# Kernel tuning notes

Measured on AMD Instinct MI355X. Metric: run time of the kernel, lower is better.

The kernel has to match this reference:

```python
import jax, jax.numpy as jnp
import numpy as np

BATCH = 64
NUM_BEAMS = 16
VOCAB = 128000
CUR_LEN = 8


def setup_inputs() -> dict:
    key = jax.random.key(0)
    k1, k2, k3 = jax.random.split(key, 3)
    rows = BATCH * NUM_BEAMS
    logits = jax.random.normal(k1, (rows, 1, VOCAB), dtype=jnp.float32)
    decoder_input_ids = jax.random.randint(k2, (rows, CUR_LEN), 0, VOCAB, dtype=jnp.int32)
    # mid-decode beam scores: arbitrary (negative-ish) cumulative log-probs
    beam_scores = jax.random.normal(k3, (rows,), dtype=jnp.float32)
    # arange(batch).repeat_interleave(num_beams) * num_beams
    beam_idx_offset = jnp.repeat(jnp.arange(BATCH, dtype=jnp.int32), NUM_BEAMS) * NUM_BEAMS
    return {
        "logits": logits,
        "decoder_input_ids": decoder_input_ids,
        "beam_scores": beam_scores,
        "beam_idx_offset": beam_idx_offset,
        "batch_size": BATCH,
        "num_beams": NUM_BEAMS,
    }


def reference(logits, decoder_input_ids, beam_scores, beam_idx_offset, batch_size, num_beams):
    # logits: [batch*beams, seq, vocab]; only the last position is used.
    vocab_size = logits.shape[-1]
    next_token_scores = jax.nn.log_softmax(logits[:, -1, :], axis=-1)  # [B*K, V]
    next_token_scores = next_token_scores + beam_scores[:, None]
    next_token_scores = next_token_scores.reshape(batch_size, num_beams * vocab_size)
    # top 2*K over the joint (beam, vocab) axis, sorted descending
    top_scores, top_idx = jax.lax.top_k(next_token_scores, 2 * num_beams)
    next_indices = top_idx // vocab_size  # source beam within batch
    next_tokens = top_idx % vocab_size    # token id
    new_beam_scores = top_scores[:, :num_beams].reshape(-1)           # [B*K]
    beam_next_tokens = next_tokens[:, :num_beams].reshape(-1)         # [B*K]
    beam_idx = next_indices[:, :num_beams].reshape(-1)                # [B*K]
    gathered = decoder_input_ids[beam_idx + beam_idx_offset, :]       # reorder beams
    new_decoder_input_ids = jnp.concatenate(
        [gathered, beam_next_tokens[:, None].astype(gathered.dtype)], axis=-1
    )
    return new_decoder_input_ids, new_beam_scores
```

## Files before the change

kernel.cpp:

```cpp
#include <hip/hip_runtime.h>
#include <cfloat>
#include <climits>

#define ROWS    1024
#define VOCABSZ 128000
#define NBEAMS  16
#define NBATCH  64
#define CURLEN  8
#define KTOP    16
#define WPB     4
#define NSTEP   125
#define TCAP    128
#define TGUARD  112
#define RCAP    768
#define RFLUSH  508
#define LOG2E   1.4426950408889634f
#define LN2     0.6931471805599453f
#define THRY    (3.30f * LOG2E)

#if __has_builtin(__builtin_amdgcn_exp2f)
#define EXP2(x) __builtin_amdgcn_exp2f(x)
#else
#define EXP2(x) exp2f(x)
#endif

__global__ __launch_bounds__(256) void k1_scan(const float* __restrict__ logits,
                                               float* __restrict__ wsS,
                                               float* __restrict__ wsV,
                                               int* __restrict__ wsI) {
    __shared__ float4 tup[WPB][TCAP];
    __shared__ int    tub[WPB][TCAP];
    __shared__ float  rbv[WPB][RCAP];
    __shared__ int    rbi[WPB][RCAP];
    __shared__ float  redS[WPB];
    __shared__ int    redC[WPB];

    const int row  = blockIdx.x;
    const int t    = threadIdx.x;
    const int w    = t >> 6;
    const int lane = t & 63;
    const float4* seg4 = reinterpret_cast<const float4*>(logits + (size_t)row * VOCABSZ);

    float s0 = 0.f, s1 = 0.f, s2 = 0.f, s3 = 0.f;
    float thr = THRY;
    int   cnt = 0;
    bool  ovf = false;

#define STEP(I, P) do {                                                        \
        const float y0 = (P).x * LOG2E, y1 = (P).y * LOG2E;                    \
        const float y2 = (P).z * LOG2E, y3 = (P).w * LOG2E;                    \
        s0 += EXP2(y0); s1 += EXP2(y1); s2 += EXP2(y2); s3 += EXP2(y3);        \
        const float mx = fmaxf(fmaxf(y0, y1), fmaxf(y2, y3));                  \
        if (__any(mx > thr)) {                                                 \
            const unsigned long long mk = __ballot(mx > thr);                  \
            const int pos = cnt + __popcll(mk & ((1ull << lane) - 1ull));      \
            if (mx > thr && pos < TCAP) {                                      \
                tup[w][pos] = make_float4(y0, y1, y2, y3);                     \
                tub[w][pos] = (I) * 1024 + t * 4;                              \
            }                                                                  \
            cnt += __popcll(mk);                                               \
            if (cnt > TGUARD) { ovf = true; thr = FLT_MAX; }                   \
        }                                                                      \
    } while (0)

    float4 A0 = seg4[0 * 256 + t];
    float4 A1 = seg4[1 * 256 + t];
    float4 A2 = seg4[2 * 256 + t];
    float4 A3 = seg4[3 * 256 + t];

    for (int g = 0; g < 31; ++g) {
        const int s4 = g * 4 + 4;
        const int i0 = (s4 + 0 < NSTEP) ? s4 + 0 : NSTEP - 1;
        const int i1 = (s4 + 1 < NSTEP) ? s4 + 1 : NSTEP - 1;
        const int i2 = (s4 + 2 < NSTEP) ? s4 + 2 : NSTEP - 1;
        const int i3 = (s4 + 3 < NSTEP) ? s4 + 3 : NSTEP - 1;
        const float4 N0 = seg4[i0 * 256 + t];
        const float4 N1 = seg4[i1 * 256 + t];
        const float4 N2 = seg4[i2 * 256 + t];
        const float4 N3 = seg4[i3 * 256 + t];

        STEP(g * 4 + 0, A0); STEP(g * 4 + 1, A1);
        STEP(g * 4 + 2, A2); STEP(g * 4 + 3, A3);

        A0 = N0; A1 = N1; A2 = N2; A3 = N3;
    }
    STEP(124, A0);
#undef STEP


    float kv = -FLT_MAX; int ki = 0;
    auto do_flush = [&](int n) {
        kv = -FLT_MAX; ki = 0;
        for (int r = 0; r < KTOP; r++) {
            float bv = -FLT_MAX; int bi = INT_MAX; int bp = -1;
            for (int e = lane; e < n; e += 64) {
                const float v  = rbv[w][e];
                const int   ii = rbi[w][e];
                if (v > bv || (v == bv && ii < bi)) { bv = v; bi = ii; bp = e; }
            }
            for (int o = 32; o > 0; o >>= 1) {
                const float ov = __shfl_xor(bv, o);
                const int   oi = __shfl_xor(bi, o);
                const int   op = __shfl_xor(bp, o);
                if (ov > bv || (ov == bv && oi < bi)) { bv = ov; bi = oi; bp = op; }
            }
            if (lane == 0 && bp >= 0) rbv[w][bp] = -FLT_MAX;
            if (lane == r) { kv = bv; ki = bi; }
            thr = bv;
        }
    };

    const int nt = (cnt < TCAP) ? cnt : TCAP;
    int above = 0;
    for (int e = lane; e < nt; e += 64) {
        const float4 v = tup[w][e];
        const int    b = tub[w][e];
        rbv[w][4 * e + 0] = v.x; rbi[w][4 * e + 0] = b + 0;
        rbv[w][4 * e + 1] = v.y; rbi[w][4 * e + 1] = b + 1;
        rbv[w][4 * e + 2] = v.z; rbi[w][4 * e + 2] = b + 2;
        rbv[w][4 * e + 3] = v.w; rbi[w][4 * e + 3] = b + 3;
        above += (v.x > THRY) + (v.y > THRY) + (v.z > THRY) + (v.w > THRY);
    }
    for (int o = 32; o > 0; o >>= 1) above += __shfl_xor(above, o);

    float s = (s0 + s1) + (s2 + s3);
    for (int o = 32; o > 0; o >>= 1) s += __shfl_xor(s, o);
    if (lane == 0) { redS[w] = s; redC[w] = ovf ? -(1 << 20) : above; }
    __syncthreads();
    if (t == 0) wsS[row] = (redS[0] + redS[1]) + (redS[2] + redS[3]);
    const int rowcnt = redC[0] + redC[1] + redC[2] + redC[3];

    int cnt4 = 4 * nt;
    if (rowcnt < KTOP) {
        thr = -FLT_MAX; cnt4 = 0;
        for (int i = 0; i < NSTEP; ++i) {
            const float4 X = seg4[i * 256 + t];
            const float ys[4] = {X.x * LOG2E, X.y * LOG2E, X.z * LOG2E, X.w * LOG2E};
            #pragma unroll
            for (int j = 0; j < 4; ++j) {
                const bool pr = ys[j] > thr;
                const unsigned long long mk = __ballot(pr);
                if (mk) {
                    const int pos = cnt4 + __popcll(mk & ((1ull << lane) - 1ull));
                    if (pr && pos < RCAP) { rbv[w][pos] = ys[j]; rbi[w][pos] = i * 1024 + t * 4 + j; }
                    cnt4 += __popcll(mk);
                    if (cnt4 > RFLUSH) {
                        do_flush(cnt4);
                        if (lane < KTOP) { rbv[w][lane] = kv; rbi[w][lane] = ki; }
                        cnt4 = KTOP;
                    }
                }
            }
        }
    }

    do_flush(cnt4);

    if (lane < KTOP) {
        wsV[(size_t)row * 64 + w * KTOP + lane] = kv;
        wsI[(size_t)row * 64 + w * KTOP + lane] = ki;
    }
}

__global__ __launch_bounds__(64) void k2_select(const float* __restrict__ wsS,
                                                const float* __restrict__ wsV,
                                                const int* __restrict__ wsI,
                                                const float* __restrict__ beam_scores,
                                                const int* __restrict__ dec_ids,
                                                const int* __restrict__ beam_idx_offset,
                                                float* __restrict__ out) {
    const int batch = blockIdx.x;
    const int lane  = threadIdx.x;

    __shared__ float LSs[NBEAMS], BSs[NBEAMS];
    if (lane < NBEAMS) {
        const int row = batch * NBEAMS + lane;
        LSs[lane] = log2f(wsS[row]);
        BSs[lane] = beam_scores[row];
    }
    __syncthreads();

    float sc[16]; int cb[16];
    #pragma unroll
    for (int p = 0; p < 16; p++) {
        const size_t base = (size_t)(batch * NBEAMS + p) * 64 + lane;
        const float v = wsV[base];
        const int idx = wsI[base];
        sc[p] = (v - LSs[p]) * LN2 + BSs[p];
        cb[p] = p * VOCABSZ + idx;
    }

    unsigned int selmask = 0;
    float fs = 0.f; int fc = 0;
    for (int r = 0; r < KTOP; r++) {
        float bv = -FLT_MAX; int bi = INT_MAX; int bslot = -1;
        #pragma unroll
        for (int p = 0; p < 16; p++) {
            const bool avail = !((selmask >> p) & 1u);
            if (avail && (sc[p] > bv || (sc[p] == bv && cb[p] < bi))) {
                bv = sc[p]; bi = cb[p]; bslot = p;
            }
        }
        int bl = lane;
        for (int o = 32; o > 0; o >>= 1) {
            const float ov  = __shfl_xor(bv, o);
            const int   oi  = __shfl_xor(bi, o);
            const int   obl = __shfl_xor(bl, o);
            const int   obs = __shfl_xor(bslot, o);
            if (ov > bv || (ov == bv && oi < bi)) { bv = ov; bi = oi; bl = obl; bslot = obs; }
        }
        if (lane == bl) selmask |= (1u << bslot);
        if (lane == r) { fs = bv; fc = bi; }
    }

    if (lane < NBEAMS) {
        const int out_row = batch * NBEAMS + lane;
        const int beam  = fc / VOCABSZ;
        const int token = fc - beam * VOCABSZ;
        float* out0 = out;
        float* out1 = out + ROWS * (CURLEN + 1);
        out1[out_row] = fs;
        const int src = beam + beam_idx_offset[out_row];
        #pragma unroll
        for (int j = 0; j < CURLEN; j++)
            out0[out_row * (CURLEN + 1) + j] = (float)dec_ids[src * CURLEN + j];
        out0[out_row * (CURLEN + 1) + CURLEN] = (float)token;
    }
}

extern "C" void kernel_launch(void* const* d_in, const int* in_sizes, int n_in,
                              void* d_out, int out_size, void* d_ws, size_t ws_size,
                              hipStream_t stream) {
    const float* logits = (const float*)d_in[0];
    const int*   dec    = (const int*)d_in[1];
    const float* bscore = (const float*)d_in[2];
    const int*   bio    = (const int*)d_in[3];

    float* ws  = (float*)d_ws;
    float* wsS = ws;
    float* wsV = ws + ROWS;
    int*   wsI = (int*)(ws + ROWS + ROWS * 64);

    k1_scan<<<ROWS, 256, 0, stream>>>(logits, wsS, wsV, wsI);
    k2_select<<<NBATCH, 64, 0, stream>>>(wsS, wsV, wsI, bscore, dec, bio,
                                         (float*)d_out);
}
```

Before: 135.5 us.

## Split each vocab row across two blocks and shrink LDS for occupancy

The scan kernel now launches two blocks per row, each covering about half the vocabulary. Each block writes its own partial exp-sum and per-wave top-16 candidates, and the select kernel sums the two partial sums and picks from 32 candidate slots per lane instead of 16. The value staging buffer is aliased onto the threshold tuple buffer, capacities are reduced, and launch bounds request 8 blocks per CU, all to raise occupancy and hide memory latency on a bandwidth-bound scan. The prefilter threshold is lowered to keep enough candidates per half-row. The trade-off is a larger workspace, more work in the select kernel, and a slightly higher chance of taking the slow fallback rescan path.

```diff
diff --git a/kernel.cpp b/kernel.cpp
--- a/kernel.cpp
+++ b/kernel.cpp
@@ -9,14 +9,15 @@
 #define CURLEN  8
 #define KTOP    16
 #define WPB     4
-#define NSTEP   125
-#define TCAP    128
-#define TGUARD  112
-#define RCAP    768
-#define RFLUSH  508
+#define SPLIT   2
+#define BASE1   64512
+#define TCAP    96
+#define TGUARD  80
+#define RCAP    (4 * TCAP)
+#define RFLUSH  320
 #define LOG2E   1.4426950408889634f
 #define LN2     0.6931471805599453f
-#define THRY    (3.30f * LOG2E)
+#define THRY    (3.10f * LOG2E)
 
 #if __has_builtin(__builtin_amdgcn_exp2f)
 #define EXP2(x) __builtin_amdgcn_exp2f(x)
@@ -24,22 +25,28 @@
 #define EXP2(x) exp2f(x)
 #endif
 
-__global__ __launch_bounds__(256) void k1_scan(const float* __restrict__ logits,
-                                               float* __restrict__ wsS,
-                                               float* __restrict__ wsV,
-                                               int* __restrict__ wsI) {
+__global__ __launch_bounds__(256, 8) void k1_scan(const float* __restrict__ logits,
+                                                  float* __restrict__ wsS,
+                                                  float* __restrict__ wsV,
+                                                  int* __restrict__ wsI) {
     __shared__ float4 tup[WPB][TCAP];
     __shared__ int    tub[WPB][TCAP];
-    __shared__ float  rbv[WPB][RCAP];
-    __shared__ int    rbi[WPB][RCAP];
+    __shared__ int    rbix[WPB][RCAP];
     __shared__ float  redS[WPB];
     __shared__ int    redC[WPB];
 
-    const int row  = blockIdx.x;
-    const int t    = threadIdx.x;
-    const int w    = t >> 6;
-    const int lane = t & 63;
-    const float4* seg4 = reinterpret_cast<const float4*>(logits + (size_t)row * VOCABSZ);
+    const int gb    = blockIdx.x;
+    const int row   = gb >> 1;
+    const int blk   = gb & 1;
+    const int ebase = blk ? BASE1 : 0;
+    const int nstep = blk ? 62 : 63;
+    const int t     = threadIdx.x;
+    const int w     = t >> 6;
+    const int lane  = t & 63;
+    const float4* seg4 = reinterpret_cast<const float4*>(
+        logits + (size_t)row * VOCABSZ + ebase);
+    float* rbv = reinterpret_cast<float*>(&tup[w][0]);
+    int*   rbi = &rbix[w][0];
 
     float s0 = 0.f, s1 = 0.f, s2 = 0.f, s3 = 0.f;
     float thr = THRY;
@@ -56,7 +63,7 @@
             const int pos = cnt + __popcll(mk & ((1ull << lane) - 1ull));      \
             if (mx > thr && pos < TCAP) {                                      \
                 tup[w][pos] = make_float4(y0, y1, y2, y3);                     \
-                tub[w][pos] = (I) * 1024 + t * 4;                              \
+                tub[w][pos] = ebase + (I) * 1024 + t * 4;                      \
             }                                                                  \
             cnt += __popcll(mk);                                               \
             if (cnt > TGUARD) { ovf = true; thr = FLT_MAX; }                   \
@@ -68,12 +75,14 @@
     float4 A2 = seg4[2 * 256 + t];
     float4 A3 = seg4[3 * 256 + t];
 
-    for (int g = 0; g < 31; ++g) {
+    const int last = nstep - 1;
+    #pragma unroll 1
+    for (int g = 0; g < 15; ++g) {
         const int s4 = g * 4 + 4;
-        const int i0 = (s4 + 0 < NSTEP) ? s4 + 0 : NSTEP - 1;
-        const int i1 = (s4 + 1 < NSTEP) ? s4 + 1 : NSTEP - 1;
-        const int i2 = (s4 + 2 < NSTEP) ? s4 + 2 : NSTEP - 1;
-        const int i3 = (s4 + 3 < NSTEP) ? s4 + 3 : NSTEP - 1;
+        const int i0 = (s4 + 0 < last) ? s4 + 0 : last;
+        const int i1 = (s4 + 1 < last) ? s4 + 1 : last;
+        const int i2 = (s4 + 2 < last) ? s4 + 2 : last;
+        const int i3 = (s4 + 3 < last) ? s4 + 3 : last;
         const float4 N0 = seg4[i0 * 256 + t];
         const float4 N1 = seg4[i1 * 256 + t];
         const float4 N2 = seg4[i2 * 256 + t];
@@ -84,7 +93,8 @@
 
         A0 = N0; A1 = N1; A2 = N2; A3 = N3;
     }
-    STEP(124, A0);
+    STEP(60, A0); STEP(61, A1);
+    if (nstep == 63) STEP(62, A2);
 #undef STEP
 
 
@@ -94,8 +104,8 @@
         for (int r = 0; r < KTOP; r++) {
             float bv = -FLT_MAX; int bi = INT_MAX; int bp = -1;
             for (int e = lane; e < n; e += 64) {
-                const float v  = rbv[w][e];
-                const int   ii = rbi[w][e];
+                const float v  = rbv[e];
+                const int   ii = rbi[e];
                 if (v > bv || (v == bv && ii < bi)) { bv = v; bi = ii; bp = e; }
             }
             for (int o = 32; o > 0; o >>= 1) {
@@ -104,7 +114,7 @@
                 const int   op = __shfl_xor(bp, o);
                 if (ov > bv || (ov == bv && oi < bi)) { bv = ov; bi = oi; bp = op; }
             }
-            if (lane == 0 && bp >= 0) rbv[w][bp] = -FLT_MAX;
+            if (lane == 0 && bp >= 0) rbv[bp] = -FLT_MAX;
             if (lane == r) { kv = bv; ki = bi; }
             thr = bv;
         }
@@ -115,11 +125,11 @@
     for (int e = lane; e < nt; e += 64) {
         const float4 v = tup[w][e];
         const int    b = tub[w][e];
-        rbv[w][4 * e + 0] = v.x; rbi[w][4 * e + 0] = b + 0;
-        rbv[w][4 * e + 1] = v.y; rbi[w][4 * e + 1] = b + 1;
-        rbv[w][4 * e + 2] = v.z; rbi[w][4 * e + 2] = b + 2;
-        rbv[w][4 * e + 3] = v.w; rbi[w][4 * e + 3] = b + 3;
         above += (v.x > THRY) + (v.y > THRY) + (v.z > THRY) + (v.w > THRY);
+        rbv[4 * e + 0] = v.x; rbi[4 * e + 0] = b + 0;
+        rbv[4 * e + 1] = v.y; rbi[4 * e + 1] = b + 1;
+        rbv[4 * e + 2] = v.z; rbi[4 * e + 2] = b + 2;
+        rbv[4 * e + 3] = v.w; rbi[4 * e + 3] = b + 3;
     }
     for (int o = 32; o > 0; o >>= 1) above += __shfl_xor(above, o);
 
@@ -127,13 +137,14 @@
     for (int o = 32; o > 0; o >>= 1) s += __shfl_xor(s, o);
     if (lane == 0) { redS[w] = s; redC[w] = ovf ? -(1 << 20) : above; }
     __syncthreads();
-    if (t == 0) wsS[row] = (redS[0] + redS[1]) + (redS[2] + redS[3]);
-    const int rowcnt = redC[0] + redC[1] + redC[2] + redC[3];
+    if (t == 0) wsS[gb] = (redS[0] + redS[1]) + (redS[2] + redS[3]);
+    const int blockcnt = redC[0] + redC[1] + redC[2] + redC[3];
 
     int cnt4 = 4 * nt;
-    if (rowcnt < KTOP) {
+    if (blockcnt < KTOP) {
         thr = -FLT_MAX; cnt4 = 0;
-        for (int i = 0; i < NSTEP; ++i) {
+        #pragma unroll 1
+        for (int i = 0; i < nstep; ++i) {
             const float4 X = seg4[i * 256 + t];
             const float ys[4] = {X.x * LOG2E, X.y * LOG2E, X.z * LOG2E, X.w * LOG2E};
             #pragma unroll
@@ -142,11 +153,11 @@
                 const unsigned long long mk = __ballot(pr);
                 if (mk) {
                     const int pos = cnt4 + __popcll(mk & ((1ull << lane) - 1ull));
-                    if (pr && pos < RCAP) { rbv[w][pos] = ys[j]; rbi[w][pos] = i * 1024 + t * 4 + j; }
+                    if (pr && pos < RCAP) { rbv[pos] = ys[j]; rbi[pos] = ebase + i * 1024 + t * 4 + j; }
                     cnt4 += __popcll(mk);
                     if (cnt4 > RFLUSH) {
                         do_flush(cnt4);
-                        if (lane < KTOP) { rbv[w][lane] = kv; rbi[w][lane] = ki; }
+                        if (lane < KTOP) { rbv[lane] = kv; rbi[lane] = ki; }
                         cnt4 = KTOP;
                     }
                 }
@@ -157,8 +168,8 @@
     do_flush(cnt4);
 
     if (lane < KTOP) {
-        wsV[(size_t)row * 64 + w * KTOP + lane] = kv;
-        wsI[(size_t)row * 64 + w * KTOP + lane] = ki;
+        wsV[(size_t)row * 128 + blk * 64 + w * KTOP + lane] = kv;
+        wsI[(size_t)row * 128 + blk * 64 + w * KTOP + lane] = ki;
     }
 }
 
@@ -175,19 +186,22 @@
     __shared__ float LSs[NBEAMS], BSs[NBEAMS];
     if (lane < NBEAMS) {
         const int row = batch * NBEAMS + lane;
-        LSs[lane] = log2f(wsS[row]);
+        LSs[lane] = log2f(wsS[row * 2] + wsS[row * 2 + 1]);
         BSs[lane] = beam_scores[row];
     }
     __syncthreads();
 
-    float sc[16]; int cb[16];
+    float sc[32]; int cb[32];
     #pragma unroll
-    for (int p = 0; p < 16; p++) {
-        const size_t base = (size_t)(batch * NBEAMS + p) * 64 + lane;
+    for (int p = 0; p < 32; p++) {
+        const int slot = p * 64 + lane;
+        const int rw   = slot >> 7;
+        const int j    = slot & 127;
+        const size_t base = (size_t)(batch * NBEAMS + rw) * 128 + j;
         const float v = wsV[base];
         const int idx = wsI[base];
-        sc[p] = (v - LSs[p]) * LN2 + BSs[p];
-        cb[p] = p * VOCABSZ + idx;
+        sc[p] = (v - LSs[rw]) * LN2 + BSs[rw];
+        cb[p] = rw * VOCABSZ + idx;
     }
 
     unsigned int selmask = 0;
@@ -195,7 +209,7 @@
     for (int r = 0; r < KTOP; r++) {
         float bv = -FLT_MAX; int bi = INT_MAX; int bslot = -1;
         #pragma unroll
-        for (int p = 0; p < 16; p++) {
+        for (int p = 0; p < 32; p++) {
             const bool avail = !((selmask >> p) & 1u);
             if (avail && (sc[p] > bv || (sc[p] == bv && cb[p] < bi))) {
                 bv = sc[p]; bi = cb[p]; bslot = p;
@@ -238,10 +252,10 @@
 
     float* ws  = (float*)d_ws;
     float* wsS = ws;
-    float* wsV = ws + ROWS;
-    int*   wsI = (int*)(ws + ROWS + ROWS * 64);
-
-    k1_scan<<<ROWS, 256, 0, stream>>>(logits, wsS, wsV, wsI);
+    float* wsV = ws + ROWS * SPLIT;
+    int*   wsI = (int*)(ws + ROWS * SPLIT + (size_t)ROWS * 128);
+
+    k1_scan<<<ROWS * SPLIT, 256, 0, stream>>>(logits, wsS, wsV, wsI);
     k2_select<<<NBATCH, 64, 0, stream>>>(wsS, wsV, wsI, bscore, dec, bio,
                                          (float*)d_out);
 }
```

Result: slower. 150.7 us (+11.2%).
